# Optimization experiments

Hardware: AMD Instinct MI355X
Metric: run time of the kernel (lower is better)

Reference implementation:

```python
import jax, jax.numpy as jnp
import numpy as np

N, M, D = 4096, 4096, 8


def setup_inputs() -> dict:
    key = jax.random.key(0)
    k1, k2 = jax.random.split(key)
    x = jax.random.normal(k1, (N, D), dtype=jnp.float32)
    xx = jax.random.normal(k2, (M, D), dtype=jnp.float32)
    # parameters stored in free (log) form; positive() == exp()
    log_scale = jnp.zeros((D,), dtype=jnp.float32)      # scale = 1.0 per dim
    log_variance = jnp.zeros((), dtype=jnp.float32)     # variance = 1.0
    return {"x": x, "xx": xx, "log_scale": log_scale, "log_variance": log_variance}


def reference(x, xx, log_scale, log_variance):
    scale = jnp.exp(log_scale)          # positive(_scale), shape [D]
    variance = jnp.exp(log_variance)    # positive(_variance), scalar (diag())
    # r: [N, M, D] broadcasted, scaled pairwise difference
    r = (x[:, None, :] - xx[None, :, :]) / scale
    # cov: [N, M] RBF kernel matrix
    cov = jnp.exp(-0.5 * jnp.sum(r * r, axis=-1)) * variance
    return cov
```

## Files before the change

### kernel.cpp

```cpp
#include <hip/hip_runtime.h>
#include <math.h>


constexpr int D    = 8;
constexpr int TJ   = 4;
constexpr int BLK  = 256;
constexpr int RPB  = 16;
constexpr int RBAT = 8;

typedef float f32x4 __attribute__((ext_vector_type(4)));

__global__ __launch_bounds__(BLK) void rbf_kernel(
    const float* __restrict__ x,
    const float* __restrict__ xx,
    const float* __restrict__ log_scale,
    const float* __restrict__ log_var,
    float* __restrict__ out,
    int N, int M)
{
    const int j0 = blockIdx.x * (BLK * TJ) + threadIdx.x * TJ;
    const int i0 = blockIdx.y * RPB;
    if (j0 + TJ > M || i0 + RPB > N) return;

    constexpr float LOG2E = 1.4426950408889634f;
    float w[D];
#pragma unroll
    for (int d = 0; d < D; ++d) {
        const float s = __expf(-log_scale[d]);
        w[d] = s * s * LOG2E;
    }
    const float lv2 = log_var[0] * LOG2E;

    float B[TJ][D], c[TJ];
#pragma unroll
    for (int jj = 0; jj < TJ; ++jj) {
        const float4* p = (const float4*)(xx + (size_t)(j0 + jj) * D);
        const float4 a = p[0], b = p[1];
        const float v[D] = {a.x, a.y, a.z, a.w, b.x, b.y, b.z, b.w};
        float q = 0.f;
#pragma unroll
        for (int d = 0; d < D; ++d) {
            B[jj][d] = v[d] * w[d];
            q = fmaf(v[d], B[jj][d], q);
        }
        c[jj] = fmaf(-0.5f, q, lv2);
    }

#pragma unroll
    for (int bat = 0; bat < RPB / RBAT; ++bat) {
        const int ib = i0 + bat * RBAT;
        float res[RBAT][TJ];

#pragma unroll
        for (int r = 0; r < RBAT; ++r) {
            const int i = ib + r;
            const float4* px = (const float4*)(x + (size_t)i * D);
            const float4 a = px[0], b = px[1];
            const float xv[D] = {a.x, a.y, a.z, a.w, b.x, b.y, b.z, b.w};
            float q = 0.f;
#pragma unroll
            for (int d = 0; d < D; ++d) q = fmaf(xv[d] * w[d], xv[d], q);
            const float h = -0.5f * q;
#pragma unroll
            for (int jj = 0; jj < TJ; ++jj) {
                float e = h + c[jj];
#pragma unroll
                for (int d = 0; d < D; ++d) e = fmaf(xv[d], B[jj][d], e);
                res[r][jj] = __builtin_amdgcn_exp2f(e);
            }
        }

#pragma unroll
        for (int r = 0; r < RBAT; ++r) {
            const f32x4 o = {res[r][0], res[r][1], res[r][2], res[r][3]};
            *(f32x4*)(out + (size_t)(ib + r) * M + j0) = o;
        }
    }
}

extern "C" void kernel_launch(void* const* d_in, const int* in_sizes, int n_in,
                              void* d_out, int out_size, void* d_ws, size_t ws_size,
                              hipStream_t stream) {
    const float* x  = (const float*)d_in[0];
    const float* xx = (const float*)d_in[1];
    const float* ls = (const float*)d_in[2];
    const float* lv = (const float*)d_in[3];
    float* out      = (float*)d_out;

    const int N = in_sizes[0] / D;
    const int M = in_sizes[1] / D;

    dim3 block(BLK, 1, 1);
    dim3 grid((M + BLK * TJ - 1) / (BLK * TJ), (N + RPB - 1) / RPB, 1);
    rbf_kernel<<<grid, block, 0, stream>>>(x, xx, ls, lv, out, N, M);
}
```

Baseline: 86.66 us.

## Use persistent grid-stride row loop with each block covering full output row

Replaces the 2D grid of row-tile blocks with 512 persistent blocks that loop over rows with a grid stride. Each thread keeps 16 xx columns (split into four strided quads) resident in registers, and every block writes a full 4096-wide row per iteration. This amortizes xx loading and weight setup across many rows and cuts block launch overhead. In exchange it uses more registers per thread (lower occupancy), exposes less ILP per row, and hardcodes M == 4096, returning early otherwise.

```diff
diff --git a/kernel.cpp b/kernel.cpp
--- a/kernel.cpp
+++ b/kernel.cpp
@@ -3,10 +3,9 @@
 
 
 constexpr int D    = 8;
-constexpr int TJ   = 4;
 constexpr int BLK  = 256;
-constexpr int RPB  = 16;
-constexpr int RBAT = 8;
+constexpr int NQ   = 4;
+constexpr int GRID = 512;
 
 typedef float f32x4 __attribute__((ext_vector_type(4)));
 
@@ -18,9 +17,8 @@
     float* __restrict__ out,
     int N, int M)
 {
-    const int j0 = blockIdx.x * (BLK * TJ) + threadIdx.x * TJ;
-    const int i0 = blockIdx.y * RPB;
-    if (j0 + TJ > M || i0 + RPB > N) return;
+    const int t = threadIdx.x;
+    if (M != BLK * 4 * NQ) return;
 
     constexpr float LOG2E = 1.4426950408889634f;
     float w[D];
@@ -31,49 +29,50 @@
     }
     const float lv2 = log_var[0] * LOG2E;
 
-    float B[TJ][D], c[TJ];
+    float B[NQ * 4][D], c[NQ * 4];
 #pragma unroll
-    for (int jj = 0; jj < TJ; ++jj) {
-        const float4* p = (const float4*)(xx + (size_t)(j0 + jj) * D);
-        const float4 a = p[0], b = p[1];
-        const float v[D] = {a.x, a.y, a.z, a.w, b.x, b.y, b.z, b.w};
+    for (int s = 0; s < NQ; ++s) {
+#pragma unroll
+        for (int k = 0; k < 4; ++k) {
+            const int j   = s * (BLK * 4) + t * 4 + k;
+            const int idx = s * 4 + k;
+            const float4* p = (const float4*)(xx + (size_t)j * D);
+            const float4 a = p[0], b = p[1];
+            const float v[D] = {a.x, a.y, a.z, a.w, b.x, b.y, b.z, b.w};
+            float q = 0.f;
+#pragma unroll
+            for (int d = 0; d < D; ++d) {
+                B[idx][d] = v[d] * w[d];
+                q = fmaf(v[d], B[idx][d], q);
+            }
+            c[idx] = fmaf(-0.5f, q, lv2);
+        }
+    }
+
+    for (int i = blockIdx.x; i < N; i += gridDim.x) {
+        const float4* px = (const float4*)(x + (size_t)i * D);
+        const float4 a = px[0], b = px[1];
+        const float xv[D] = {a.x, a.y, a.z, a.w, b.x, b.y, b.z, b.w};
         float q = 0.f;
 #pragma unroll
-        for (int d = 0; d < D; ++d) {
-            B[jj][d] = v[d] * w[d];
-            q = fmaf(v[d], B[jj][d], q);
-        }
-        c[jj] = fmaf(-0.5f, q, lv2);
-    }
+        for (int d = 0; d < D; ++d) q = fmaf(xv[d] * w[d], xv[d], q);
+        const float h = -0.5f * q;
 
+        float res[NQ * 4];
 #pragma unroll
-    for (int bat = 0; bat < RPB / RBAT; ++bat) {
-        const int ib = i0 + bat * RBAT;
-        float res[RBAT][TJ];
-
+        for (int idx = 0; idx < NQ * 4; ++idx) {
+            float e = h + c[idx];
 #pragma unroll
-        for (int r = 0; r < RBAT; ++r) {
-            const int i = ib + r;
-            const float4* px = (const float4*)(x + (size_t)i * D);
-            const float4 a = px[0], b = px[1];
-            const float xv[D] = {a.x, a.y, a.z, a.w, b.x, b.y, b.z, b.w};
-            float q = 0.f;
-#pragma unroll
-            for (int d = 0; d < D; ++d) q = fmaf(xv[d] * w[d], xv[d], q);
-            const float h = -0.5f * q;
-#pragma unroll
-            for (int jj = 0; jj < TJ; ++jj) {
-                float e = h + c[jj];
-#pragma unroll
-                for (int d = 0; d < D; ++d) e = fmaf(xv[d], B[jj][d], e);
-                res[r][jj] = __builtin_amdgcn_exp2f(e);
-            }
+            for (int d = 0; d < D; ++d) e = fmaf(xv[d], B[idx][d], e);
+            res[idx] = __builtin_amdgcn_exp2f(e);
         }
 
+        float* rowp = out + (size_t)i * M;
 #pragma unroll
-        for (int r = 0; r < RBAT; ++r) {
-            const f32x4 o = {res[r][0], res[r][1], res[r][2], res[r][3]};
-            *(f32x4*)(out + (size_t)(ib + r) * M + j0) = o;
+        for (int s = 0; s < NQ; ++s) {
+            const f32x4 o = {res[s * 4 + 0], res[s * 4 + 1],
+                             res[s * 4 + 2], res[s * 4 + 3]};
+            *(f32x4*)(rowp + s * (BLK * 4) + t * 4) = o;
         }
     }
 }
@@ -91,6 +90,6 @@
     const int M = in_sizes[1] / D;
 
     dim3 block(BLK, 1, 1);
-    dim3 grid((M + BLK * TJ - 1) / (BLK * TJ), (N + RPB - 1) / RPB, 1);
+    dim3 grid(GRID, 1, 1);
     rbf_kernel<<<grid, block, 0, stream>>>(x, xx, ls, lv, out, N, M);
 }
```

After: 89.66 us. +3.5%, slower.
